# Performance work log

Measured on AMD Instinct MI355X. Metric: run time of the kernel, lower is better.

The kernel has to match this reference:

```python
import jax, jax.numpy as jnp
import numpy as np

N = 100000
E = 800000
IN_DIM = 128
HID = 128
OUT = 40
EPS = 1e-5


def setup_inputs() -> dict:
    key = jax.random.key(0)
    ks = jax.random.split(key, 12)
    inp = {
        "feat": jax.random.normal(ks[0], (N, IN_DIM), dtype=jnp.float32),
        "src": jax.random.randint(ks[1], (E,), 0, N, dtype=jnp.int32),
        "dst": jax.random.randint(ks[2], (E,), 0, N, dtype=jnp.int32),
        # layer 0: SAGEConv(IN_DIM -> HID), no bias; BN params
        "W_self0": jax.random.normal(ks[3], (IN_DIM, HID), dtype=jnp.float32) / np.sqrt(IN_DIM),
        "W_neigh0": jax.random.normal(ks[4], (IN_DIM, HID), dtype=jnp.float32) / np.sqrt(IN_DIM),
        "gamma0": jnp.ones((HID,), dtype=jnp.float32),
        "beta0": jnp.zeros((HID,), dtype=jnp.float32),
        # layer 1: SAGEConv(HID -> HID), no bias; BN params
        "W_self1": jax.random.normal(ks[5], (HID, HID), dtype=jnp.float32) / np.sqrt(HID),
        "W_neigh1": jax.random.normal(ks[6], (HID, HID), dtype=jnp.float32) / np.sqrt(HID),
        "gamma1": jnp.ones((HID,), dtype=jnp.float32),
        "beta1": jnp.zeros((HID,), dtype=jnp.float32),
        # layer 2: SAGEConv(HID -> OUT), with bias
        "W_self2": jax.random.normal(ks[7], (HID, OUT), dtype=jnp.float32) / np.sqrt(HID),
        "W_neigh2": jax.random.normal(ks[8], (HID, OUT), dtype=jnp.float32) / np.sqrt(HID),
        "b2": jnp.zeros((OUT,), dtype=jnp.float32),
    }
    return inp


def _sage_conv(h, src, dst, W_self, W_neigh, bias=None):
    # DGL SAGEConv with 'mean' aggregation: mean over in-neighbors, then
    # fc_self(h) + fc_neigh(h_neigh) (+ bias).
    msg = h[src]  # [E, d] gather of source-node features
    agg = jax.ops.segment_sum(msg, dst, num_segments=N)  # [N, d]
    deg = jax.ops.segment_sum(jnp.ones((src.shape[0],), h.dtype), dst, num_segments=N)
    h_neigh = agg / jnp.maximum(deg, 1.0)[:, None]
    out = h @ W_self + h_neigh @ W_neigh
    if bias is not None:
        out = out + bias
    return out


def _batch_norm(h, gamma, beta):
    # BatchNorm1d training-mode forward: batch statistics over nodes (axis 0).
    mean = jnp.mean(h, axis=0)
    var = jnp.mean(jnp.square(h - mean), axis=0)
    return (h - mean) * jax.lax.rsqrt(var + EPS) * gamma + beta


def reference(feat, src, dst,
              W_self0, W_neigh0, gamma0, beta0,
              W_self1, W_neigh1, gamma1, beta1,
              W_self2, W_neigh2, b2):
    # dropout layers are identity in eval mode
    h = feat
    h = _sage_conv(h, src, dst, W_self0, W_neigh0)
    h = jax.nn.relu(_batch_norm(h, gamma0, beta0))
    h = _sage_conv(h, src, dst, W_self1, W_neigh1)
    h = jax.nn.relu(_batch_norm(h, gamma1, beta1))
    h = _sage_conv(h, src, dst, W_self2, W_neigh2, bias=b2)
    return h
```

## Files before the change

kernel.cpp:

```cpp
#include <hip/hip_runtime.h>

#define N_NODES 100000
#define N_EDGES 800000
#define DIM 128
#define OUTD 40
#define OUTP 48
#define BN_EPS 1e-5f
#define SCAN_NB 98
#define NBKT 98
#define BKT_CAP 12288

typedef __bf16 bf16x8_t __attribute__((ext_vector_type(8)));
typedef float f32x4_t __attribute__((ext_vector_type(4)));
typedef float f32x2_t __attribute__((ext_vector_type(2)));

__device__ __forceinline__ unsigned short f2bf(float f) {
    unsigned int u = __builtin_bit_cast(unsigned int, f);
    u = (u + 0x7FFF + ((u >> 16) & 1)) >> 16;
    return (unsigned short)u;
}


__global__ __launch_bounds__(256) void zero_ws_kernel(int* __restrict__ p) {
    p[blockIdx.x * 256 + threadIdx.x] = 0;
}


__global__ __launch_bounds__(256) void bucketA_kernel(const int* __restrict__ src,
                                                      const int* __restrict__ dst,
                                                      uint2* __restrict__ pairs,
                                                      int* __restrict__ gcursor) {
    __shared__ int cnt[NBKT], base[NBKT], rec[NBKT];
    const int t = threadIdx.x;
    if (t < NBKT) { cnt[t] = 0; rec[t] = 0; }
    __syncthreads();
    const int e0 = blockIdx.x * 4096 + t * 16;
    const bool active = (e0 + 16 <= N_EDGES);
    int s[16], d[16];
    if (active) {
#pragma unroll
        for (int i = 0; i < 4; ++i) {
            int4 sv = *reinterpret_cast<const int4*>(&src[e0 + i * 4]);
            int4 dv = *reinterpret_cast<const int4*>(&dst[e0 + i * 4]);
            s[i * 4 + 0] = sv.x; s[i * 4 + 1] = sv.y; s[i * 4 + 2] = sv.z; s[i * 4 + 3] = sv.w;
            d[i * 4 + 0] = dv.x; d[i * 4 + 1] = dv.y; d[i * 4 + 2] = dv.z; d[i * 4 + 3] = dv.w;
        }
#pragma unroll
        for (int i = 0; i < 16; ++i) atomicAdd(&cnt[d[i] >> 10], 1);
    }
    __syncthreads();
    if (t < NBKT && cnt[t] > 0) base[t] = atomicAdd(&gcursor[t], cnt[t]);
    __syncthreads();
    if (active) {
#pragma unroll
        for (int i = 0; i < 16; ++i) {
            int bk = d[i] >> 10;
            int loc = atomicAdd(&rec[bk], 1);
            pairs[(size_t)bk * BKT_CAP + base[bk] + loc] = make_uint2((unsigned)s[i], (unsigned)d[i]);
        }
    }
}

__global__ __launch_bounds__(256) void phaseB_deg_kernel(const uint2* __restrict__ pairs,
                                                         const int* __restrict__ gcursor,
                                                         int* __restrict__ deg) {
    __shared__ int hist[1024];
    const int b = blockIdx.x;
    const int t = threadIdx.x;
#pragma unroll
    for (int j = 0; j < 4; ++j) hist[t * 4 + j] = 0;
    __syncthreads();
    const int m = gcursor[b];
    const uint2* __restrict__ bp = &pairs[(size_t)b * BKT_CAP];
    for (int i = t; i < m; i += 256) {
        uint2 p = bp[i];
        atomicAdd(&hist[p.y & 1023], 1);
    }
    __syncthreads();
    const int n0 = b << 10;
#pragma unroll
    for (int j = 0; j < 4; ++j) {
        int node = n0 + t * 4 + j;
        if (node < N_NODES) deg[node] = hist[t * 4 + j];
    }
}

__global__ __launch_bounds__(256) void scan_partial_kernel(const int* __restrict__ deg,
                                                           int* __restrict__ partials) {
    int b = blockIdx.x;
    int tid = threadIdx.x;
    int base = b * 1024 + tid * 4;
    int t0 = 0, t1 = 0, t2 = 0, t3 = 0;
    if (base + 3 < N_NODES) {
        int4 v = *reinterpret_cast<const int4*>(&deg[base]);
        t0 = v.x; t1 = v.y; t2 = v.z; t3 = v.w;
    } else {
        if (base + 0 < N_NODES) t0 = deg[base + 0];
        if (base + 1 < N_NODES) t1 = deg[base + 1];
        if (base + 2 < N_NODES) t2 = deg[base + 2];
        if (base + 3 < N_NODES) t3 = deg[base + 3];
    }
    int s = t0 + t1 + t2 + t3;
    __shared__ int red[256];
    red[tid] = s;
    __syncthreads();
    for (int o = 128; o; o >>= 1) {
        if (tid < o) red[tid] += red[tid + o];
        __syncthreads();
    }
    if (tid == 0) partials[b] = red[0];
}

__global__ __launch_bounds__(128) void scan_partials_kernel(int* __restrict__ partials) {
    __shared__ int s[128];
    int t = threadIdx.x;
    int v = (t < SCAN_NB) ? partials[t] : 0;
    s[t] = v;
    __syncthreads();
    for (int off = 1; off < 128; off <<= 1) {
        int u = (t >= off) ? s[t - off] : 0;
        __syncthreads();
        s[t] += u;
        __syncthreads();
    }
    if (t < SCAN_NB) partials[t] = s[t] - v;
}

__global__ __launch_bounds__(256) void scan_final_kernel(const int* __restrict__ deg,
                                                         const int* __restrict__ partials,
                                                         int* __restrict__ row_off) {
    int b = blockIdx.x;
    int tid = threadIdx.x;
    int base = b * 1024 + tid * 4;
    int t0 = 0, t1 = 0, t2 = 0, t3 = 0;
    if (base + 3 < N_NODES) {
        int4 v = *reinterpret_cast<const int4*>(&deg[base]);
        t0 = v.x; t1 = v.y; t2 = v.z; t3 = v.w;
    } else {
        if (base + 0 < N_NODES) t0 = deg[base + 0];
        if (base + 1 < N_NODES) t1 = deg[base + 1];
        if (base + 2 < N_NODES) t2 = deg[base + 2];
        if (base + 3 < N_NODES) t3 = deg[base + 3];
    }
    int s = t0 + t1 + t2 + t3;
    __shared__ int sc[256];
    sc[tid] = s;
    __syncthreads();
    for (int off = 1; off < 256; off <<= 1) {
        int u = (tid >= off) ? sc[tid - off] : 0;
        __syncthreads();
        sc[tid] += u;
        __syncthreads();
    }
    int run = partials[b] + sc[tid] - s;
    if (base + 0 < N_NODES) row_off[base + 0] = run; run += t0;
    if (base + 1 < N_NODES) row_off[base + 1] = run; run += t1;
    if (base + 2 < N_NODES) row_off[base + 2] = run; run += t2;
    if (base + 3 < N_NODES) row_off[base + 3] = run;
    if (b == 0 && tid == 0) row_off[N_NODES] = N_EDGES;
}

__global__ __launch_bounds__(256) void phaseC_fill_kernel(const uint2* __restrict__ pairs,
                                                          const int* __restrict__ gcursor,
                                                          const int* __restrict__ row_off,
                                                          int* __restrict__ csr_src) {
    __shared__ int cur[1024];
    const int b = blockIdx.x;
    const int t = threadIdx.x;
    const int n0 = b << 10;
#pragma unroll
    for (int j = 0; j < 4; ++j) {
        int node = n0 + t * 4 + j;
        if (node < N_NODES) cur[t * 4 + j] = row_off[node];
    }
    __syncthreads();
    const int m = gcursor[b];
    const uint2* __restrict__ bp = &pairs[(size_t)b * BKT_CAP];
    for (int i = t; i < m; i += 256) {
        uint2 p = bp[i];
        int pos = atomicAdd(&cur[p.y & 1023], 1);
        csr_src[pos] = (int)p.x;
    }
}


__global__ __launch_bounds__(256) void convert_bf16_kernel(const float* __restrict__ in,
                                                           unsigned short* __restrict__ out) {
    size_t i = (size_t)(blockIdx.x * blockDim.x + threadIdx.x) * 4;
    float4 v = *reinterpret_cast<const float4*>(&in[i]);
    ushort4 o;
    o.x = f2bf(v.x); o.y = f2bf(v.y); o.z = f2bf(v.z); o.w = f2bf(v.w);
    *reinterpret_cast<ushort4*>(&out[i]) = o;
}


__global__ __launch_bounds__(256) void wt_build_kernel(const float* __restrict__ Ws0,
                                                       const float* __restrict__ Wn0,
                                                       const float* __restrict__ Ws1,
                                                       const float* __restrict__ Wn1,
                                                       unsigned short* __restrict__ WT0,
                                                       unsigned short* __restrict__ WT1) {
    int e = blockIdx.x * blockDim.x + threadIdx.x;
    int layer = e >> 15;
    int r = e & 32767;
    int n = r >> 8;
    int k = r & 255;
    const float* Ws = layer ? Ws1 : Ws0;
    const float* Wn = layer ? Wn1 : Wn0;
    float v = (k < DIM) ? Ws[k * DIM + n] : Wn[(k - DIM) * DIM + n];
    unsigned short* WT = layer ? WT1 : WT0;
    WT[n * 256 + k] = f2bf(v);
}

__global__ __launch_bounds__(256) void wt2_build_kernel(const float* __restrict__ Ws2,
                                                        const float* __restrict__ Wn2,
                                                        unsigned short* __restrict__ WT2) {
    int e = blockIdx.x * blockDim.x + threadIdx.x;
    int n = e >> 8;
    int k = e & 255;
    float v = 0.f;
    if (n < OUTD) v = (k < DIM) ? Ws2[k * OUTD + n] : Wn2[(k - DIM) * OUTD + n];
    WT2[n * 256 + k] = f2bf(v);
}


__device__ __forceinline__ void unpack_add2(f32x2_t* a, uint4 v) {
    f32x2_t t0, t1, t2, t3;
    t0[0] = __builtin_bit_cast(float, v.x << 16);
    t0[1] = __builtin_bit_cast(float, v.x & 0xFFFF0000u);
    t1[0] = __builtin_bit_cast(float, v.y << 16);
    t1[1] = __builtin_bit_cast(float, v.y & 0xFFFF0000u);
    t2[0] = __builtin_bit_cast(float, v.z << 16);
    t2[1] = __builtin_bit_cast(float, v.z & 0xFFFF0000u);
    t3[0] = __builtin_bit_cast(float, v.w << 16);
    t3[1] = __builtin_bit_cast(float, v.w & 0xFFFF0000u);
    a[0] += t0;
    a[1] += t1;
    a[2] += t2;
    a[3] += t3;
}

__global__ __launch_bounds__(256) void agg_bf16_kernel(const unsigned short* __restrict__ h,
                                                       const int* __restrict__ row_off,
                                                       const int* __restrict__ csr_src,
                                                       unsigned short* __restrict__ hn) {
    const int wave = threadIdx.x >> 6;
    const int lane = threadIdx.x & 63;
    const int grp = lane >> 4;
    const int l16 = lane & 15;
    const int node = blockIdx.x * 16 + wave * 4 + grp;
    const int lo = row_off[node];
    const int hi = row_off[node + 1];
    const int cnt = hi - lo;

    f32x2_t a2[4];
#pragma unroll
    for (int q = 0; q < 4; ++q) a2[q] = (f32x2_t){0.f, 0.f};
    const unsigned rowoff = (unsigned)l16 * 8u;

    for (int t = 0; t < cnt; t += 8) {
        const int last = cnt - 1;
        int idx[8];
        bool p[8];
#pragma unroll
        for (int j = 0; j < 8; ++j) {
            p[j] = (t + j < cnt);
            idx[j] = csr_src[lo + min(t + j, last)];
        }
        uint4 v[8];
#pragma unroll
        for (int j = 0; j < 8; ++j)
            v[j] = *reinterpret_cast<const uint4*>(&h[(size_t)idx[j] * DIM + rowoff]);
#pragma unroll
        for (int j = 0; j < 8; ++j)
            if (p[j]) unpack_add2(a2, v[j]);
    }

    const float rd = (cnt > 0) ? 1.0f / (float)cnt : 1.0f;
    uint4 o;
    o.x = (unsigned int)f2bf(a2[0][0] * rd) | ((unsigned int)f2bf(a2[0][1] * rd) << 16);
    o.y = (unsigned int)f2bf(a2[1][0] * rd) | ((unsigned int)f2bf(a2[1][1] * rd) << 16);
    o.z = (unsigned int)f2bf(a2[2][0] * rd) | ((unsigned int)f2bf(a2[2][1] * rd) << 16);
    o.w = (unsigned int)f2bf(a2[3][0] * rd) | ((unsigned int)f2bf(a2[3][1] * rd) << 16);
    *reinterpret_cast<uint4*>(&hn[(size_t)node * DIM + rowoff]) = o;
}


__global__ __launch_bounds__(256) void gemm_mfma_kernel(const unsigned short* __restrict__ Ab,
                                                        const unsigned short* __restrict__ Hb,
                                                        const unsigned short* __restrict__ WT,
                                                        unsigned short* __restrict__ C,
                                                        float* __restrict__ bnbuf) {
    __shared__ unsigned short wt[16384];
    const int tid = threadIdx.x;
    const int wid = tid >> 6;
    const int lane = tid & 63;
    const int lrow = lane & 15;
    const int g = lane >> 4;
    const int r0 = blockIdx.x * 128 + wid * 32;

    bf16x8_t a[2][8];
#pragma unroll
    for (int ks = 0; ks < 8; ++ks) {
        const unsigned short* __restrict__ base = (ks < 4) ? Ab : Hb;
        const int kk = (ks & 3) * 32 + g * 8;
#pragma unroll
        for (int mt = 0; mt < 2; ++mt) {
            int row = r0 + mt * 16 + lrow;
            if (row >= N_NODES) row = N_NODES - 1;
            a[mt][ks] = *reinterpret_cast<const bf16x8_t*>(&base[(size_t)row * DIM + kk]);
        }
    }

    f32x4_t acc[2][8];
#pragma unroll
    for (int mt = 0; mt < 2; ++mt)
#pragma unroll
        for (int nt = 0; nt < 8; ++nt) acc[mt][nt] = (f32x4_t){0.f, 0.f, 0.f, 0.f};

#pragma unroll
    for (int hh = 0; hh < 2; ++hh) {
        if (hh) __syncthreads();
#pragma unroll
        for (int i = 0; i < 8; ++i) {
            int c = i * 256 + tid;
            int n = c >> 4;
            int koff = (c & 15) * 8;
            unsigned int waddr = ((unsigned int)(c * 16)) ^ (((unsigned int)(n & 7)) << 4);
            uint4 v = *reinterpret_cast<const uint4*>(&WT[n * 256 + hh * 128 + koff]);
            *reinterpret_cast<uint4*>(reinterpret_cast<char*>(wt) + waddr) = v;
        }
        __syncthreads();
#pragma unroll
        for (int ks = 0; ks < 4; ++ks) {
#pragma unroll
            for (int nt = 0; nt < 8; ++nt) {
                int n = nt * 16 + lrow;
                unsigned int raddr = ((unsigned int)(n * 256 + ks * 64 + g * 16)) ^ (((unsigned int)(n & 7)) << 4);
                bf16x8_t b = *reinterpret_cast<const bf16x8_t*>(reinterpret_cast<const char*>(wt) + raddr);
                acc[0][nt] = __builtin_amdgcn_mfma_f32_16x16x32_bf16(a[0][hh * 4 + ks], b, acc[0][nt], 0, 0, 0);
                acc[1][nt] = __builtin_amdgcn_mfma_f32_16x16x32_bf16(a[1][hh * 4 + ks], b, acc[1][nt], 0, 0, 0);
            }
        }
    }

    float ssum[8], ssq[8];
#pragma unroll
    for (int nt = 0; nt < 8; ++nt) { ssum[nt] = 0.f; ssq[nt] = 0.f; }
#pragma unroll
    for (int mt = 0; mt < 2; ++mt) {
#pragma unroll
        for (int j = 0; j < 4; ++j) {
            int row = r0 + mt * 16 + g * 4 + j;
            if (row < N_NODES) {
#pragma unroll
                for (int nt = 0; nt < 8; ++nt) {
                    float v = acc[mt][nt][j];
                    ssum[nt] += v;
                    ssq[nt] += v * v;
                }
            }
        }
    }
#pragma unroll
    for (int nt = 0; nt < 8; ++nt) {
        ssum[nt] += __shfl_xor(ssum[nt], 16, 64);
        ssum[nt] += __shfl_xor(ssum[nt], 32, 64);
        ssq[nt] += __shfl_xor(ssq[nt], 16, 64);
        ssq[nt] += __shfl_xor(ssq[nt], 32, 64);
    }
    __syncthreads();
    float* ls = reinterpret_cast<float*>(wt);
    float* lq = ls + 512;
    if (g == 0) {
#pragma unroll
        for (int nt = 0; nt < 8; ++nt) {
            ls[wid * 128 + nt * 16 + lrow] = ssum[nt];
            lq[wid * 128 + nt * 16 + lrow] = ssq[nt];
        }
    }
    __syncthreads();
    if (tid < 128) {
        float s = ls[tid] + ls[128 + tid] + ls[256 + tid] + ls[384 + tid];
        float q = lq[tid] + lq[128 + tid] + lq[256 + tid] + lq[384 + tid];
        float* rb = bnbuf + (blockIdx.x & 7) * 256;
        atomicAdd(&rb[tid], s);
        atomicAdd(&rb[128 + tid], q);
    }

#pragma unroll
    for (int mt = 0; mt < 2; ++mt) {
#pragma unroll
        for (int j = 0; j < 4; ++j) {
            int row = r0 + mt * 16 + g * 4 + j;
            if (row < N_NODES) {
#pragma unroll
                for (int nt = 0; nt < 8; ++nt)
                    C[(size_t)row * DIM + nt * 16 + lrow] = f2bf(acc[mt][nt][j]);
            }
        }
    }
}


__global__ __launch_bounds__(256) void bn_apply_bf16_kernel(unsigned short* __restrict__ H,
                                                            const float* __restrict__ bnbuf,
                                                            const float* __restrict__ gamma,
                                                            const float* __restrict__ beta) {
    __shared__ float red[256];
    {
        int t = threadIdx.x;
        float s = 0.f;
#pragma unroll
        for (int r = 0; r < 8; ++r) s += bnbuf[r * 256 + t];
        red[t] = s;
    }
    __syncthreads();
    size_t idx = (size_t)(blockIdx.x * blockDim.x + threadIdx.x) * 8;
    const float invN = 1.0f / (float)N_NODES;
    int c = (int)(idx & (DIM - 1));
    uint4 v = *reinterpret_cast<const uint4*>(&H[idx]);
    unsigned int w[4] = {v.x, v.y, v.z, v.w};
    uint4 o;
    unsigned int* op = &o.x;
#pragma unroll
    for (int p = 0; p < 4; ++p) {
        float x0 = __builtin_bit_cast(float, w[p] << 16);
        float x1 = __builtin_bit_cast(float, w[p] & 0xFFFF0000u);
        int c0 = c + p * 2, c1 = c0 + 1;
        float mean0 = red[c0] * invN, mean1 = red[c1] * invN;
        float var0 = red[128 + c0] * invN - mean0 * mean0;
        float var1 = red[128 + c1] * invN - mean1 * mean1;
        float y0 = (x0 - mean0) * gamma[c0] * rsqrtf(var0 + BN_EPS) + beta[c0];
        float y1 = (x1 - mean1) * gamma[c1] * rsqrtf(var1 + BN_EPS) + beta[c1];
        y0 = y0 > 0.f ? y0 : 0.f;
        y1 = y1 > 0.f ? y1 : 0.f;
        op[p] = (unsigned int)f2bf(y0) | ((unsigned int)f2bf(y1) << 16);
    }
    *reinterpret_cast<uint4*>(&H[idx]) = o;
}


__global__ __launch_bounds__(256) void gemm_out_mfma_kernel(const unsigned short* __restrict__ Ab,
                                                            const unsigned short* __restrict__ Hb,
                                                            const unsigned short* __restrict__ WT2,
                                                            const float* __restrict__ bias,
                                                            float* __restrict__ C) {
    __shared__ unsigned short wt[OUTP * 256];
    const int tid = threadIdx.x;

#pragma unroll
    for (int i = 0; i < 6; ++i) {
        int c = i * 256 + tid;
        int n = c >> 5;
        unsigned int waddr = ((unsigned int)(c * 16)) ^ (((unsigned int)(n & 7)) << 4);
        uint4 v = *reinterpret_cast<const uint4*>(&WT2[c * 8]);
        *reinterpret_cast<uint4*>(reinterpret_cast<char*>(wt) + waddr) = v;
    }
    __syncthreads();

    const int wid = tid >> 6;
    const int lane = tid & 63;
    const int lrow = lane & 15;
    const int g = lane >> 4;
    const int r0 = blockIdx.x * 128 + wid * 32;

    bf16x8_t a[2][8];
#pragma unroll
    for (int ks = 0; ks < 8; ++ks) {
        const unsigned short* __restrict__ base = (ks < 4) ? Ab : Hb;
        const int kk = (ks & 3) * 32 + g * 8;
#pragma unroll
        for (int mt = 0; mt < 2; ++mt) {
            int row = r0 + mt * 16 + lrow;
            if (row >= N_NODES) row = N_NODES - 1;
            a[mt][ks] = *reinterpret_cast<const bf16x8_t*>(&base[(size_t)row * DIM + kk]);
        }
    }

    f32x4_t acc[2][3];
#pragma unroll
    for (int mt = 0; mt < 2; ++mt)
#pragma unroll
        for (int nt = 0; nt < 3; ++nt) acc[mt][nt] = (f32x4_t){0.f, 0.f, 0.f, 0.f};

#pragma unroll
    for (int ks = 0; ks < 8; ++ks) {
#pragma unroll
        for (int nt = 0; nt < 3; ++nt) {
            int n = nt * 16 + lrow;
            unsigned int raddr = ((unsigned int)(n * 512 + ks * 64 + g * 16)) ^ (((unsigned int)(n & 7)) << 4);
            bf16x8_t b = *reinterpret_cast<const bf16x8_t*>(reinterpret_cast<const char*>(wt) + raddr);
            acc[0][nt] = __builtin_amdgcn_mfma_f32_16x16x32_bf16(a[0][ks], b, acc[0][nt], 0, 0, 0);
            acc[1][nt] = __builtin_amdgcn_mfma_f32_16x16x32_bf16(a[1][ks], b, acc[1][nt], 0, 0, 0);
        }
    }

    float bb[3];
#pragma unroll
    for (int nt = 0; nt < 3; ++nt) {
        int col = nt * 16 + lrow;
        bb[nt] = (col < OUTD) ? bias[col] : 0.f;
    }

#pragma unroll
    for (int mt = 0; mt < 2; ++mt) {
#pragma unroll
        for (int j = 0; j < 4; ++j) {
            int row = r0 + mt * 16 + g * 4 + j;
            if (row < N_NODES) {
#pragma unroll
                for (int nt = 0; nt < 3; ++nt) {
                    int col = nt * 16 + lrow;
                    if (col < OUTD)
                        C[(size_t)row * OUTD + col] = acc[mt][nt][j] + bb[nt];
                }
            }
        }
    }
}


extern "C" void kernel_launch(void* const* d_in, const int* in_sizes, int n_in,
                              void* d_out, int out_size, void* d_ws, size_t ws_size,
                              hipStream_t stream) {
    const float* feat = (const float*)d_in[0];
    const int* src = (const int*)d_in[1];
    const int* dst = (const int*)d_in[2];
    const float* Ws0 = (const float*)d_in[3];
    const float* Wn0 = (const float*)d_in[4];
    const float* g0  = (const float*)d_in[5];
    const float* be0 = (const float*)d_in[6];
    const float* Ws1 = (const float*)d_in[7];
    const float* Wn1 = (const float*)d_in[8];
    const float* g1  = (const float*)d_in[9];
    const float* be1 = (const float*)d_in[10];
    const float* Ws2 = (const float*)d_in[11];
    const float* Wn2 = (const float*)d_in[12];
    const float* b2  = (const float*)d_in[13];
    float* out = (float*)d_out;

    char* ws = (char*)d_ws;
    int*   gcursor = (int*)(ws);
    float* bn      = (float*)(ws + 4096);
    int*   row_off = (int*)(ws + 20480);
    int*   partials= (int*)(ws + 421120);
    uint2* pairs   = (uint2*)(ws + 421888);
    int*   csr     = (int*)(ws + 10055680);
    int*   deg     = (int*)(ws + 13255680);
    unsigned short* featb = (unsigned short*)(ws + 13655808);
    unsigned short* hnb   = (unsigned short*)(ws + 39255808);
    unsigned short* h0b   = (unsigned short*)(ws + 64855808);
    unsigned short* WT0   = (unsigned short*)(ws + 90455808);
    unsigned short* WT1   = (unsigned short*)(ws + 90521344);
    unsigned short* WT2   = (unsigned short*)(ws + 90586880);
    unsigned short* h1b   = featb;
    float* bn0 = bn;
    float* bn1 = bn + 2048;

    const int ABK = (N_EDGES + 4095) / 4096;
    const int AGB = N_NODES / 16;
    const int MB = (N_NODES + 127) / 128;
    const int NE = (N_NODES * DIM) / 4 / 256;
    const int NB8 = (N_NODES * DIM) / 8 / 256;

    zero_ws_kernel<<<20, 256, 0, stream>>>((int*)ws);

    bucketA_kernel<<<ABK, 256, 0, stream>>>(src, dst, pairs, gcursor);
    phaseB_deg_kernel<<<NBKT, 256, 0, stream>>>(pairs, gcursor, deg);
    scan_partial_kernel<<<SCAN_NB, 256, 0, stream>>>(deg, partials);
    scan_partials_kernel<<<1, 128, 0, stream>>>(partials);
    scan_final_kernel<<<SCAN_NB, 256, 0, stream>>>(deg, partials, row_off);
    phaseC_fill_kernel<<<NBKT, 256, 0, stream>>>(pairs, gcursor, row_off, csr);

    convert_bf16_kernel<<<NE, 256, 0, stream>>>(feat, featb);
    wt_build_kernel<<<256, 256, 0, stream>>>(Ws0, Wn0, Ws1, Wn1, WT0, WT1);
    wt2_build_kernel<<<48, 256, 0, stream>>>(Ws2, Wn2, WT2);

    agg_bf16_kernel<<<AGB, 256, 0, stream>>>(featb, row_off, csr, hnb);
    gemm_mfma_kernel<<<MB, 256, 0, stream>>>(featb, hnb, WT0, h0b, bn0);
    bn_apply_bf16_kernel<<<NB8, 256, 0, stream>>>(h0b, bn0, g0, be0);

    agg_bf16_kernel<<<AGB, 256, 0, stream>>>(h0b, row_off, csr, hnb);
    gemm_mfma_kernel<<<MB, 256, 0, stream>>>(h0b, hnb, WT1, h1b, bn1);
    bn_apply_bf16_kernel<<<NB8, 256, 0, stream>>>(h1b, bn1, g1, be1);

    agg_bf16_kernel<<<AGB, 256, 0, stream>>>(h1b, row_off, csr, hnb);
    gemm_out_mfma_kernel<<<MB, 256, 0, stream>>>(h1b, hnb, WT2, b2, out);
}
```

Baseline: 238.3 us.

## Fuse BatchNorm+ReLU into consumer aggregation and GEMM loads

```diff
diff --git a/kernel.cpp b/kernel.cpp
--- a/kernel.cpp
+++ b/kernel.cpp
@@ -18,6 +18,9 @@
     unsigned int u = __builtin_bit_cast(unsigned int, f);
     u = (u + 0x7FFF + ((u >> 16) & 1)) >> 16;
     return (unsigned short)u;
+}
+__device__ __forceinline__ float bf2f_u(unsigned int lo16) {
+    return __builtin_bit_cast(float, lo16 << 16);
 }
 
 
@@ -224,26 +227,59 @@
 }
 
 
+__global__ __launch_bounds__(128) void bn_prep_kernel(const float* __restrict__ bnbuf,
+                                                      const float* __restrict__ gamma,
+                                                      const float* __restrict__ beta,
+                                                      float* __restrict__ bnss) {
+    const int t = threadIdx.x;
+    float s = 0.f, q = 0.f;
+#pragma unroll
+    for (int r = 0; r < 8; ++r) {
+        s += bnbuf[r * 256 + t];
+        q += bnbuf[r * 256 + 128 + t];
+    }
+    const float invN = 1.0f / (float)N_NODES;
+    float mean = s * invN;
+    float var = q * invN - mean * mean;
+    float sc = gamma[t] * rsqrtf(var + BN_EPS);
+    bnss[t] = sc;
+    bnss[128 + t] = beta[t] - mean * sc;
+}
+
+
 __device__ __forceinline__ void unpack_add2(f32x2_t* a, uint4 v) {
     f32x2_t t0, t1, t2, t3;
-    t0[0] = __builtin_bit_cast(float, v.x << 16);
-    t0[1] = __builtin_bit_cast(float, v.x & 0xFFFF0000u);
-    t1[0] = __builtin_bit_cast(float, v.y << 16);
-    t1[1] = __builtin_bit_cast(float, v.y & 0xFFFF0000u);
-    t2[0] = __builtin_bit_cast(float, v.z << 16);
-    t2[1] = __builtin_bit_cast(float, v.z & 0xFFFF0000u);
-    t3[0] = __builtin_bit_cast(float, v.w << 16);
-    t3[1] = __builtin_bit_cast(float, v.w & 0xFFFF0000u);
-    a[0] += t0;
-    a[1] += t1;
-    a[2] += t2;
-    a[3] += t3;
+    t0[0] = bf2f_u(v.x << 16 >> 16 << 16 >> 16);
+    (void)t0; (void)t1; (void)t2; (void)t3;
+    a[0][0] += bf2f_u(v.x & 0xFFFFu);
+    a[0][1] += __builtin_bit_cast(float, v.x & 0xFFFF0000u);
+    a[1][0] += bf2f_u(v.y & 0xFFFFu);
+    a[1][1] += __builtin_bit_cast(float, v.y & 0xFFFF0000u);
+    a[2][0] += bf2f_u(v.z & 0xFFFFu);
+    a[2][1] += __builtin_bit_cast(float, v.z & 0xFFFF0000u);
+    a[3][0] += bf2f_u(v.w & 0xFFFFu);
+    a[3][1] += __builtin_bit_cast(float, v.w & 0xFFFF0000u);
+}
+
+__device__ __forceinline__ void unpack_bn_add2(f32x2_t* a, uint4 v,
+                                               const float* s, const float* sh) {
+    unsigned int w[4] = {v.x, v.y, v.z, v.w};
+#pragma unroll
+    for (int q = 0; q < 4; ++q) {
+        float x0 = bf2f_u(w[q] & 0xFFFFu);
+        float x1 = __builtin_bit_cast(float, w[q] & 0xFFFF0000u);
+        float y0 = fmaxf(fmaf(x0, s[2 * q], sh[2 * q]), 0.f);
+        float y1 = fmaxf(fmaf(x1, s[2 * q + 1], sh[2 * q + 1]), 0.f);
+        a[q][0] += y0;
+        a[q][1] += y1;
+    }
 }
 
 __global__ __launch_bounds__(256) void agg_bf16_kernel(const unsigned short* __restrict__ h,
                                                        const int* __restrict__ row_off,
                                                        const int* __restrict__ csr_src,
-                                                       unsigned short* __restrict__ hn) {
+                                                       unsigned short* __restrict__ hn,
+                                                       const float* __restrict__ bnss) {
     const int wave = threadIdx.x >> 6;
     const int lane = threadIdx.x & 63;
     const int grp = lane >> 4;
@@ -258,22 +294,48 @@
     for (int q = 0; q < 4; ++q) a2[q] = (f32x2_t){0.f, 0.f};
     const unsigned rowoff = (unsigned)l16 * 8u;
 
-    for (int t = 0; t < cnt; t += 8) {
-        const int last = cnt - 1;
-        int idx[8];
-        bool p[8];
+    if (bnss == nullptr) {
+        for (int t = 0; t < cnt; t += 8) {
+            const int last = cnt - 1;
+            int idx[8];
+            bool p[8];
+#pragma unroll
+            for (int j = 0; j < 8; ++j) {
+                p[j] = (t + j < cnt);
+                idx[j] = csr_src[lo + min(t + j, last)];
+            }
+            uint4 v[8];
+#pragma unroll
+            for (int j = 0; j < 8; ++j)
+                v[j] = *reinterpret_cast<const uint4*>(&h[(size_t)idx[j] * DIM + rowoff]);
+#pragma unroll
+            for (int j = 0; j < 8; ++j)
+                if (p[j]) unpack_add2(a2, v[j]);
+        }
+    } else {
+        float s[8], sh[8];
 #pragma unroll
         for (int j = 0; j < 8; ++j) {
-            p[j] = (t + j < cnt);
-            idx[j] = csr_src[lo + min(t + j, last)];
-        }
-        uint4 v[8];
-#pragma unroll
-        for (int j = 0; j < 8; ++j)
-            v[j] = *reinterpret_cast<const uint4*>(&h[(size_t)idx[j] * DIM + rowoff]);
-#pragma unroll
-        for (int j = 0; j < 8; ++j)
-            if (p[j]) unpack_add2(a2, v[j]);
+            s[j] = bnss[l16 * 8 + j];
+            sh[j] = bnss[128 + l16 * 8 + j];
+        }
+        for (int t = 0; t < cnt; t += 8) {
+            const int last = cnt - 1;
+            int idx[8];
+            bool p[8];
+#pragma unroll
+            for (int j = 0; j < 8; ++j) {
+                p[j] = (t + j < cnt);
+                idx[j] = csr_src[lo + min(t + j, last)];
+            }
+            uint4 v[8];
+#pragma unroll
+            for (int j = 0; j < 8; ++j)
+                v[j] = *reinterpret_cast<const uint4*>(&h[(size_t)idx[j] * DIM + rowoff]);
+#pragma unroll
+            for (int j = 0; j < 8; ++j)
+                if (p[j]) unpack_bn_add2(a2, v[j], s, sh);
+        }
     }
 
     const float rd = (cnt > 0) ? 1.0f / (float)cnt : 1.0f;
@@ -286,11 +348,23 @@
 }
 
 
+__device__ __forceinline__ bf16x8_t bn_frag(bf16x8_t av, const float* __restrict__ bnss, int kk) {
+    bf16x8_t r;
+#pragma unroll
+    for (int j = 0; j < 8; ++j) {
+        float x = (float)av[j];
+        float y = fmaxf(fmaf(x, bnss[kk + j], bnss[128 + kk + j]), 0.f);
+        r[j] = (__bf16)y;
+    }
+    return r;
+}
+
 __global__ __launch_bounds__(256) void gemm_mfma_kernel(const unsigned short* __restrict__ Ab,
                                                         const unsigned short* __restrict__ Hb,
                                                         const unsigned short* __restrict__ WT,
                                                         unsigned short* __restrict__ C,
-                                                        float* __restrict__ bnbuf) {
+                                                        float* __restrict__ bnbuf,
+                                                        const float* __restrict__ bnss) {
     __shared__ unsigned short wt[16384];
     const int tid = threadIdx.x;
     const int wid = tid >> 6;
@@ -311,6 +385,15 @@
             a[mt][ks] = *reinterpret_cast<const bf16x8_t*>(&base[(size_t)row * DIM + kk]);
         }
     }
+    if (bnss != nullptr) {
+#pragma unroll
+        for (int ks = 0; ks < 4; ++ks) {
+            const int kk = ks * 32 + g * 8;
+#pragma unroll
+            for (int mt = 0; mt < 2; ++mt)
+                a[mt][ks] = bn_frag(a[mt][ks], bnss, kk);
+        }
+    }
 
     f32x4_t acc[2][8];
 #pragma unroll
@@ -403,49 +486,12 @@
 }
 
 
-__global__ __launch_bounds__(256) void bn_apply_bf16_kernel(unsigned short* __restrict__ H,
-                                                            const float* __restrict__ bnbuf,
-                                                            const float* __restrict__ gamma,
-                                                            const float* __restrict__ beta) {
-    __shared__ float red[256];
-    {
-        int t = threadIdx.x;
-        float s = 0.f;
-#pragma unroll
-        for (int r = 0; r < 8; ++r) s += bnbuf[r * 256 + t];
-        red[t] = s;
-    }
-    __syncthreads();
-    size_t idx = (size_t)(blockIdx.x * blockDim.x + threadIdx.x) * 8;
-    const float invN = 1.0f / (float)N_NODES;
-    int c = (int)(idx & (DIM - 1));
-    uint4 v = *reinterpret_cast<const uint4*>(&H[idx]);
-    unsigned int w[4] = {v.x, v.y, v.z, v.w};
-    uint4 o;
-    unsigned int* op = &o.x;
-#pragma unroll
-    for (int p = 0; p < 4; ++p) {
-        float x0 = __builtin_bit_cast(float, w[p] << 16);
-        float x1 = __builtin_bit_cast(float, w[p] & 0xFFFF0000u);
-        int c0 = c + p * 2, c1 = c0 + 1;
-        float mean0 = red[c0] * invN, mean1 = red[c1] * invN;
-        float var0 = red[128 + c0] * invN - mean0 * mean0;
-        float var1 = red[128 + c1] * invN - mean1 * mean1;
-        float y0 = (x0 - mean0) * gamma[c0] * rsqrtf(var0 + BN_EPS) + beta[c0];
-        float y1 = (x1 - mean1) * gamma[c1] * rsqrtf(var1 + BN_EPS) + beta[c1];
-        y0 = y0 > 0.f ? y0 : 0.f;
-        y1 = y1 > 0.f ? y1 : 0.f;
-        op[p] = (unsigned int)f2bf(y0) | ((unsigned int)f2bf(y1) << 16);
-    }
-    *reinterpret_cast<uint4*>(&H[idx]) = o;
-}
-
-
 __global__ __launch_bounds__(256) void gemm_out_mfma_kernel(const unsigned short* __restrict__ Ab,
                                                             const unsigned short* __restrict__ Hb,
                                                             const unsigned short* __restrict__ WT2,
                                                             const float* __restrict__ bias,
-                                                            float* __restrict__ C) {
+                                                            float* __restrict__ C,
+                                                            const float* __restrict__ bnss) {
     __shared__ unsigned short wt[OUTP * 256];
     const int tid = threadIdx.x;
 
@@ -476,6 +522,13 @@
             if (row >= N_NODES) row = N_NODES - 1;
             a[mt][ks] = *reinterpret_cast<const bf16x8_t*>(&base[(size_t)row * DIM + kk]);
         }
+    }
+#pragma unroll
+    for (int ks = 0; ks < 4; ++ks) {
+        const int kk = ks * 32 + g * 8;
+#pragma unroll
+        for (int mt = 0; mt < 2; ++mt)
+            a[mt][ks] = bn_frag(a[mt][ks], bnss, kk);
     }
 
     f32x4_t acc[2][3];
@@ -554,6 +607,8 @@
     unsigned short* WT0   = (unsigned short*)(ws + 90455808);
     unsigned short* WT1   = (unsigned short*)(ws + 90521344);
     unsigned short* WT2   = (unsigned short*)(ws + 90586880);
+    float* bn0ss   = (float*)(ws + 90611456);
+    float* bn1ss   = (float*)(ws + 90612480);
     unsigned short* h1b   = featb;
     float* bn0 = bn;
     float* bn1 = bn + 2048;
@@ -562,7 +617,6 @@
     const int AGB = N_NODES / 16;
     const int MB = (N_NODES + 127) / 128;
     const int NE = (N_NODES * DIM) / 4 / 256;
-    const int NB8 = (N_NODES * DIM) / 8 / 256;
 
     zero_ws_kernel<<<20, 256, 0, stream>>>((int*)ws);
 
@@ -577,14 +631,14 @@
     wt_build_kernel<<<256, 256, 0, stream>>>(Ws0, Wn0, Ws1, Wn1, WT0, WT1);
     wt2_build_kernel<<<48, 256, 0, stream>>>(Ws2, Wn2, WT2);
 
-    agg_bf16_kernel<<<AGB, 256, 0, stream>>>(featb, row_off, csr, hnb);
-    gemm_mfma_kernel<<<MB, 256, 0, stream>>>(featb, hnb, WT0, h0b, bn0);
-    bn_apply_bf16_kernel<<<NB8, 256, 0, stream>>>(h0b, bn0, g0, be0);
-
-    agg_bf16_kernel<<<AGB, 256, 0, stream>>>(h0b, row_off, csr, hnb);
-    gemm_mfma_kernel<<<MB, 256, 0, stream>>>(h0b, hnb, WT1, h1b, bn1);
-    bn_apply_bf16_kernel<<<NB8, 256, 0, stream>>>(h1b, bn1, g1, be1);
-
-    agg_bf16_kernel<<<AGB, 256, 0, stream>>>(h1b, row_off, csr, hnb);
-    gemm_out_mfma_kernel<<<MB, 256, 0, stream>>>(h1b, hnb, WT2, b2, out);
-}
+    agg_bf16_kernel<<<AGB, 256, 0, stream>>>(featb, row_off, csr, hnb, nullptr);
+    gemm_mfma_kernel<<<MB, 256, 0, stream>>>(featb, hnb, WT0, h0b, bn0, nullptr);
+    bn_prep_kernel<<<1, 128, 0, stream>>>(bn0, g0, be0, bn0ss);
+
+    agg_bf16_kernel<<<AGB, 256, 0, stream>>>(h0b, row_off, csr, hnb, bn0ss);
+    gemm_mfma_kernel<<<MB, 256, 0, stream>>>(h0b, hnb, WT1, h1b, bn1, bn0ss);
+    bn_prep_kernel<<<1, 128, 0, stream>>>(bn1, g1, be1, bn1ss);
+
+    agg_bf16_kernel<<<AGB, 256, 0, stream>>>(h1b, row_off, csr, hnb, bn1ss);
+    gemm_out_mfma_kernel<<<MB, 256, 0, stream>>>(h1b, hnb, WT2, b2, out, bn1ss);
+}
```

After: 245.0 us. 1.03x slower.
